# Optimization experiments

Measured on AMD Instinct MI355X. Metric: run time of the kernel, lower is better.

## Reference

```python
import jax, jax.numpy as jnp
import numpy as np

T, N, D = 64, 40, 4
H, R, K = 256, 64, 2
E = N * (N - 1)


def _xavier(key, shape):
    std = (2.0 / (shape[0] + shape[1])) ** 0.5
    return (std * jax.random.normal(key, shape)).astype(jnp.float32)


def setup_inputs() -> dict:
    ks = iter(jax.random.split(jax.random.key(0), 40))
    send, recv = np.where(np.ones((N, N)) - np.eye(N))  # fully-connected directed graph, E = N*(N-1)
    p = {}
    p['inputs'] = jax.random.normal(next(ks), (1, T, N, D), dtype=jnp.float32)
    p['node_masks'] = jnp.ones((1, T, N), dtype=jnp.float32)
    p['send_edges'] = jnp.asarray(send, dtype=jnp.int32)
    p['recv_edges'] = jnp.asarray(recv, dtype=jnp.int32)
    for name, nin in (('mlp1', D), ('mlp2', 2 * H), ('mlp3', H), ('mlp4', 3 * H)):
        p[name + '_W1'] = _xavier(next(ks), (H, nin))
        p[name + '_b1'] = jnp.full((H,), 0.1, jnp.float32)
        p[name + '_W2'] = _xavier(next(ks), (H, H))
        p[name + '_b2'] = jnp.full((H,), 0.1, jnp.float32)
    s = float(1.0 / np.sqrt(R))
    for nm in ('fwd', 'rev'):
        p[nm + '_Wih'] = jax.random.uniform(next(ks), (4 * R, H), jnp.float32, -s, s)
        p[nm + '_Whh'] = jax.random.uniform(next(ks), (4 * R, R), jnp.float32, -s, s)
        p[nm + '_bih'] = jnp.zeros((4 * R,), jnp.float32)
        p[nm + '_bhh'] = jnp.zeros((4 * R,), jnp.float32)
    p['enc_W'] = _xavier(next(ks), (K, 2 * R))
    p['enc_b'] = jnp.full((K,), 0.1, jnp.float32)
    p['prior_W'] = _xavier(next(ks), (K, R))
    p['prior_b'] = jnp.full((K,), 0.1, jnp.float32)
    return p


def _mlp(x, W1, b1, W2, b2):
    # RefNRIMLP in eval mode with no_bn=True: elu(fc2(elu(fc1(x))))
    return jax.nn.elu(jax.nn.elu(x @ W1.T + b1) @ W2.T + b2)


def _lstm(xs, Wih, Whh, bih, bhh):
    # xs: [T, E, H] -> hidden states [T, E, R]; PyTorch LSTM gate order i, f, g, o
    def step(carry, xt):
        h, c = carry
        g = xt @ Wih.T + bih + h @ Whh.T + bhh
        i, f, gg, o = jnp.split(g, 4, axis=-1)
        c = jax.nn.sigmoid(f) * c + jax.nn.sigmoid(i) * jnp.tanh(gg)
        h = jax.nn.sigmoid(o) * jnp.tanh(c)
        return (h, c), h
    Rh = Whh.shape[1]
    init = (jnp.zeros((xs.shape[1], Rh), xs.dtype), jnp.zeros((xs.shape[1], Rh), xs.dtype))
    _, hs = jax.lax.scan(step, init, xs)
    return hs


def _encode(inputs, send, recv,
            m1W1, m1b1, m1W2, m1b2, m2W1, m2b1, m2W2, m2b2,
            m3W1, m3b1, m3W2, m3b2, m4W1, m4b1, m4W2, m4b2,
            fWih, fWhh, fbih, fbhh, rWih, rWhh, rbih, rbhh,
            encW, encb, priW, prib):
    x = inputs[0]                                                  # [T, N, D]
    h = _mlp(x, m1W1, m1b1, m1W2, m1b2)                            # [T, N, H]
    e = jnp.concatenate([h[:, send], h[:, recv]], axis=-1)         # node2edge gather [T, E, 2H]
    e = _mlp(e, m2W1, m2b1, m2W2, m2b2)                            # [T, E, H]
    skip = e
    n = jnp.zeros((x.shape[0], x.shape[1], e.shape[-1]), e.dtype)
    n = n.at[:, recv].add(e)                                       # edge2node scatter-add (index_add_)
    n = _mlp(n, m3W1, m3b1, m3W2, m3b2)                            # [T, N, H]
    e = jnp.concatenate([n[:, send], n[:, recv], skip], axis=-1)   # [T, E, 3H]
    e = _mlp(e, m4W1, m4b1, m4W2, m4b2)                            # per-edge features over time [T, E, H]
    fwd_h = _lstm(e, fWih, fWhh, fbih, fbhh)                       # [T, E, R]
    rev_h = _lstm(e[::-1], rWih, rWhh, rbih, rbhh)[::-1]           # [T, E, R]
    prior = fwd_h @ priW.T + prib                                  # [T, E, K]
    enc = jnp.concatenate([fwd_h, rev_h], axis=-1) @ encW.T + encb # [T, E, K]
    return jnp.concatenate([prior, enc], axis=-1)                  # [T, E, 2K]


def reference(inputs, node_masks, send_edges, recv_edges,
              mlp1_W1, mlp1_b1, mlp1_W2, mlp1_b2,
              mlp2_W1, mlp2_b1, mlp2_W2, mlp2_b2,
              mlp3_W1, mlp3_b1, mlp3_W2, mlp3_b2,
              mlp4_W1, mlp4_b1, mlp4_W2, mlp4_b2,
              fwd_Wih, fwd_Whh, fwd_bih, fwd_bhh,
              rev_Wih, rev_Whh, rev_bih, rev_bhh,
              enc_W, enc_b, prior_W, prior_b):
    del node_masks  # all nodes present -> static fully-connected graph each step
    return _encode(inputs, send_edges, recv_edges,
                   mlp1_W1, mlp1_b1, mlp1_W2, mlp1_b2,
                   mlp2_W1, mlp2_b1, mlp2_W2, mlp2_b2,
                   mlp3_W1, mlp3_b1, mlp3_W2, mlp3_b2,
                   mlp4_W1, mlp4_b1, mlp4_W2, mlp4_b2,
                   fwd_Wih, fwd_Whh, fwd_bih, fwd_bhh,
                   rev_Wih, rev_Whh, rev_bih, rev_bhh,
                   enc_W, enc_b, prior_W, prior_b)
```

## Files before the change

kernel.cpp:

```cpp
#include <hip/hip_runtime.h>
#include <math.h>

#define T_ 64
#define N_ 40
#define D_ 4
#define H_ 256
#define R_ 64
#define E_ 1560
#define TE_ (T_*E_)
#define TN_ (T_*N_)

typedef unsigned short us;
typedef short short8 __attribute__((ext_vector_type(8)));
typedef float f32x4 __attribute__((ext_vector_type(4)));

__device__ __forceinline__ float elu_f(float x){ return x > 0.f ? x : (__expf(x) - 1.f); }
__device__ __forceinline__ float sig_f(float x){ return 1.f/(1.f+__expf(-x)); }
__device__ __forceinline__ float tanh_f(float x){ return 2.f/(1.f+__expf(-2.f*x)) - 1.f; }
__device__ __forceinline__ float dot4(float4 a, float4 b){ return a.x*b.x + a.y*b.y + a.z*b.z + a.w*b.w; }

__device__ __forceinline__ float bf2f(us u){ return __uint_as_float(((unsigned int)u) << 16); }
__device__ __forceinline__ us f2bf(float f){
    unsigned int u = __float_as_uint(f);
    u += 0x7FFFu + ((u >> 16) & 1u);
    return (us)(u >> 16);
}
__device__ __forceinline__ float4 ld4f(const float* p){ return *(const float4*)p; }
__device__ __forceinline__ float4 ld4f(const us* p){
    ushort4 v = *(const ushort4*)p;
    return make_float4(bf2f(v.x), bf2f(v.y), bf2f(v.z), bf2f(v.w));
}
__device__ __forceinline__ void st4f(float* p, float4 v){ *(float4*)p = v; }
__device__ __forceinline__ void st4f(us* p, float4 v){
    ushort4 o; o.x = f2bf(v.x); o.y = f2bf(v.y); o.z = f2bf(v.z); o.w = f2bf(v.w);
    *(ushort4*)p = o;
}

__device__ __forceinline__ void gld16(void* lds, const void* g){
    __builtin_amdgcn_global_load_lds((const __attribute__((address_space(1))) unsigned int*)g,
                                     (__attribute__((address_space(3))) unsigned int*)lds,
                                     16, 0, 0);
}

__device__ __forceinline__ void wsplit1(const float* W, us* hi, us* lo, int i){
    const float w = W[i];
    const us h = f2bf(w);
    hi[i] = h;
    lo[i] = f2bf(w - bf2f(h));
}

__global__ __launch_bounds__(256)
void wsplit_all(const float* __restrict__ s0, us* h0, us* l0,
                const float* __restrict__ s1, us* h1, us* l1,
                const float* __restrict__ s2, us* h2, us* l2,
                const float* __restrict__ s3, us* h3, us* l3,
                const float* __restrict__ s4, us* h4, us* l4,
                const float* __restrict__ s5, us* h5, us* l5,
                const float* __restrict__ s6, us* h6, us* l6,
                const float* __restrict__ s7, us* h7, us* l7)
{
    int i = blockIdx.x * 256 + threadIdx.x;
    if (i < 131072) { wsplit1(s0, h0, l0, i); return; } i -= 131072;
    if (i <  65536) { wsplit1(s1, h1, l1, i); return; } i -=  65536;
    if (i < 196608) { wsplit1(s2, h2, l2, i); return; } i -= 196608;
    if (i <  65536) { wsplit1(s3, h3, l3, i); return; } i -=  65536;
    if (i <  65536) { wsplit1(s4, h4, l4, i); return; } i -=  65536;
    if (i <  65536) { wsplit1(s5, h5, l5, i); return; } i -=  65536;
    if (i <  16384) { wsplit1(s6, h6, l6, i); return; } i -=  16384;
    wsplit1(s7, h7, l7, i);
}

__global__ __launch_bounds__(256)
void mlp1_kernel(const float* __restrict__ x,
                 const float* __restrict__ W1, const float* __restrict__ b1,
                 const float* __restrict__ W2, const float* __restrict__ b2,
                 us* __restrict__ hout)
{
    __shared__ float xs[8][4];
    __shared__ float h1[8][256];
    const int tid = threadIdx.x;
    const int r0  = blockIdx.x * 8;

    if (tid < 32) xs[tid >> 2][tid & 3] = x[r0 * 4 + tid];
    __syncthreads();

    const float4 w1 = *(const float4*)&W1[tid * 4];
    const float bb1 = b1[tid];
    #pragma unroll
    for (int row = 0; row < 8; ++row) {
        float v = bb1 + xs[row][0]*w1.x + xs[row][1]*w1.y + xs[row][2]*w1.z + xs[row][3]*w1.w;
        h1[row][tid] = elu_f(v);
    }
    __syncthreads();

    float acc[8];
    const float bb2 = b2[tid];
    #pragma unroll
    for (int row = 0; row < 8; ++row) acc[row] = bb2;
    const float* w2row = W2 + (size_t)tid * 256;
    for (int k4 = 0; k4 < 64; ++k4) {
        const float4 w = *(const float4*)&w2row[k4 * 4];
        #pragma unroll
        for (int row = 0; row < 8; ++row) {
            const float4 hh = *(const float4*)&h1[row][k4 * 4];
            acc[row] += dot4(hh, w);
        }
    }
    #pragma unroll
    for (int row = 0; row < 8; ++row)
        hout[(size_t)(r0 + row) * 256 + tid] = f2bf(elu_f(acc[row]));
}

template<int MODE, bool DOELU>
__global__ __launch_bounds__(256)
void gemm_mfma(const us* __restrict__ A, const us* __restrict__ A2, const us* __restrict__ A3,
               const us* __restrict__ Whi, const us* __restrict__ Wlo,
               const float* __restrict__ bias1, const float* __restrict__ bias2,
               const int* __restrict__ send, const int* __restrict__ recv,
               us* __restrict__ C, int Kdim,
               const us* __restrict__ Whi2, const us* __restrict__ Wlo2,
               const float* __restrict__ bias1b, const float* __restrict__ bias2b,
               us* __restrict__ C2)
{
    __shared__ char smem[49152];

    const int tid  = threadIdx.x;
    const int lane = tid & 63;
    const int w    = tid >> 6;
    const int ml   = lane & 15;
    const int q    = lane >> 4;
    const int bx   = blockIdx.x;
    int by         = blockIdx.y;
    const int eh   = w >> 1;
    const int fh   = w & 1;

    if (MODE == 0 && C2 != nullptr && by >= 2) {
        Whi = Whi2; Wlo = Wlo2; bias1 = bias1b; bias2 = bias2b; C = C2; by -= 2;
    }

    const int srow0 = w * 32 + (lane >> 2);
    const int srow1 = srow0 + 16;
    const int cofs  = (lane & 3) * 8;

    const int gr0 = bx * 128 + srow0, gr1 = bx * 128 + srow1;
    const us *pA0a=nullptr,*pA1a=nullptr,*pA2a=nullptr;
    const us *pA0b=nullptr,*pA1b=nullptr,*pA2b=nullptr;
    if (MODE == 0) {
        pA0a = A + (size_t)gr0 * Kdim;
        pA0b = A + (size_t)gr1 * Kdim;
    } else {
        const int t0 = gr0 / E_, e0 = gr0 - t0 * E_;
        const int t1 = gr1 / E_, e1 = gr1 - t1 * E_;
        pA0a = A  + ((size_t)(t0 * N_ + send[e0])) * H_;
        pA1a = A2 + ((size_t)(t0 * N_ + recv[e0])) * H_;
        pA0b = A  + ((size_t)(t1 * N_ + send[e1])) * H_;
        pA1b = A2 + ((size_t)(t1 * N_ + recv[e1])) * H_;
        if (MODE == 2) { pA2a = A3 + (size_t)gr0 * H_; pA2b = A3 + (size_t)gr1 * H_; }
    }
    const us* pWh0 = Whi + (size_t)(by * 128 + srow0) * Kdim;
    const us* pWh1 = Whi + (size_t)(by * 128 + srow1) * Kdim;
    const us* pWl0 = Wlo + (size_t)(by * 128 + srow0) * Kdim;
    const us* pWl1 = Wlo + (size_t)(by * 128 + srow1) * Kdim;

    f32x4 acc[4][4];
    #pragma unroll
    for (int i = 0; i < 4; ++i)
        #pragma unroll
        for (int j = 0; j < 4; ++j)
            acc[i][j] = (f32x4){0.f, 0.f, 0.f, 0.f};

    auto stage = [&](int k0, char* base) {
        const us *sa, *sb;
        if (MODE == 0) { sa = pA0a + k0; sb = pA0b + k0; }
        else if (MODE == 1) {
            sa = (k0 < 256) ? pA0a + k0 : pA1a + (k0 - 256);
            sb = (k0 < 256) ? pA0b + k0 : pA1b + (k0 - 256);
        } else {
            sa = (k0 < 256) ? pA0a + k0 : (k0 < 512) ? pA1a + (k0 - 256) : pA2a + (k0 - 512);
            sb = (k0 < 256) ? pA0b + k0 : (k0 < 512) ? pA1b + (k0 - 256) : pA2b + (k0 - 512);
        }
        gld16(base + w * 2048,                sa + cofs);
        gld16(base + w * 2048 + 1024,         sb + cofs);
        gld16(base + 8192  + w * 2048,        pWh0 + k0 + cofs);
        gld16(base + 8192  + w * 2048 + 1024, pWh1 + k0 + cofs);
        gld16(base + 16384 + w * 2048,        pWl0 + k0 + cofs);
        gld16(base + 16384 + w * 2048 + 1024, pWl1 + k0 + cofs);
    };

    stage(0, smem);
    const int nk = Kdim >> 5;
    for (int k = 0; k < nk; ++k) {
        char* cur = smem + (k & 1) * 24576;
        char* nxt = smem + ((k + 1) & 1) * 24576;
        __builtin_amdgcn_s_barrier();
        if (k + 1 < nk) {
            stage((k + 1) * 32, nxt);
            __builtin_amdgcn_s_waitcnt(0x3F76);
        } else {
            __builtin_amdgcn_s_waitcnt(0x3F70);
        }
        __builtin_amdgcn_s_barrier();

        short8 wh[4], wl[4], ef[4];
        #pragma unroll
        for (int mt = 0; mt < 4; ++mt) {
            const int fr = fh * 64 + mt * 16 + ml;
            wh[mt] = *(const short8*)(cur + 8192  + fr * 64 + q * 16);
            wl[mt] = *(const short8*)(cur + 16384 + fr * 64 + q * 16);
        }
        #pragma unroll
        for (int nt = 0; nt < 4; ++nt) {
            const int er = eh * 64 + nt * 16 + ml;
            ef[nt] = *(const short8*)(cur + er * 64 + q * 16);
        }
        #pragma unroll
        for (int mt = 0; mt < 4; ++mt)
            #pragma unroll
            for (int nt = 0; nt < 4; ++nt) {
                acc[mt][nt] = __builtin_amdgcn_mfma_f32_16x16x32_bf16(wh[mt], ef[nt], acc[mt][nt], 0, 0, 0);
                acc[mt][nt] = __builtin_amdgcn_mfma_f32_16x16x32_bf16(wl[mt], ef[nt], acc[mt][nt], 0, 0, 0);
            }
    }

    #pragma unroll
    for (int mt = 0; mt < 4; ++mt) {
        const int colb = by * 128 + fh * 64 + mt * 16 + q * 4;
        float4 bb = *(const float4*)(bias1 + colb);
        if (bias2) {
            const float4 b2 = *(const float4*)(bias2 + colb);
            bb.x += b2.x; bb.y += b2.y; bb.z += b2.z; bb.w += b2.w;
        }
        #pragma unroll
        for (int nt = 0; nt < 4; ++nt) {
            const int row = bx * 128 + eh * 64 + nt * 16 + ml;
            float4 v;
            v.x = acc[mt][nt][0] + bb.x; v.y = acc[mt][nt][1] + bb.y;
            v.z = acc[mt][nt][2] + bb.z; v.w = acc[mt][nt][3] + bb.w;
            if (DOELU) { v.x = elu_f(v.x); v.y = elu_f(v.y); v.z = elu_f(v.z); v.w = elu_f(v.w); }
            ushort4 o; o.x = f2bf(v.x); o.y = f2bf(v.y); o.z = f2bf(v.z); o.w = f2bf(v.w);
            *(ushort4*)(C + (size_t)row * 256 + colb) = o;
        }
    }
}

template<bool DOELU, typename TA, typename TC>
__global__ __launch_bounds__(256)
void gemm_nt(const TA* __restrict__ A, const float* __restrict__ W,
             const float* __restrict__ bias1,
             TC* __restrict__ C, int M, int Kdim)
{
    __shared__ float As[16][64];
    __shared__ float Ws[16][64];

    const int tid = threadIdx.x;
    const int am  = tid >> 2;
    const int ak  = (tid & 3) * 4;
    const int gm  = blockIdx.x * 64 + am;

    const TA* aptr0 = A + (size_t)gm * Kdim;
    const float* wptr = W + (size_t)(blockIdx.y * 64 + am) * Kdim;

    const int tx = tid & 15, ty = tid >> 4;
    float acc[4][4] = {};

    for (int k0 = 0; k0 < Kdim; k0 += 16) {
        const float4 a4 = ld4f(aptr0 + k0 + ak);
        const float4 w4 = *(const float4*)(wptr + k0 + (tid & 3) * 4);

        __syncthreads();
        As[ak+0][am] = a4.x; As[ak+1][am] = a4.y; As[ak+2][am] = a4.z; As[ak+3][am] = a4.w;
        const int wk = (tid & 3) * 4;
        Ws[wk+0][am] = w4.x; Ws[wk+1][am] = w4.y; Ws[wk+2][am] = w4.z; Ws[wk+3][am] = w4.w;
        __syncthreads();

        #pragma unroll
        for (int kq = 0; kq < 16; ++kq) {
            const float4 av = *(const float4*)&As[kq][ty * 4];
            const float4 wv = *(const float4*)&Ws[kq][tx * 4];
            const float a_[4] = {av.x, av.y, av.z, av.w};
            const float w_[4] = {wv.x, wv.y, wv.z, wv.w};
            #pragma unroll
            for (int i = 0; i < 4; ++i)
                #pragma unroll
                for (int j = 0; j < 4; ++j)
                    acc[i][j] += a_[i] * w_[j];
        }
    }

    const int gn = blockIdx.y * 64 + tx * 4;
    const float4 bb = *(const float4*)&bias1[gn];
    #pragma unroll
    for (int i = 0; i < 4; ++i) {
        const int row = blockIdx.x * 64 + ty * 4 + i;
        float4 o;
        o.x = acc[i][0] + bb.x; o.y = acc[i][1] + bb.y;
        o.z = acc[i][2] + bb.z; o.w = acc[i][3] + bb.w;
        if (DOELU) { o.x = elu_f(o.x); o.y = elu_f(o.y); o.z = elu_f(o.z); o.w = elu_f(o.w); }
        st4f(C + (size_t)row * 256 + gn, o);
    }
}

__global__ __launch_bounds__(256)
void aggregate_kernel(const us* __restrict__ eSkip, const int* __restrict__ recv,
                      float* __restrict__ nAgg)
{
    const int t = blockIdx.x / N_;
    const int j = blockIdx.x - t * N_;
    const int c = threadIdx.x;
    const us* basep = eSkip + (size_t)t * E_ * H_ + c;
    float acc = 0.f;
    #pragma unroll
    for (int s = 0; s < N_; ++s) {
        if (s == j) continue;
        const int e = s * (N_ - 1) + (j < s ? j : j - 1);
        acc += bf2f(basep[(size_t)e * H_]);
    }
    nAgg[(size_t)blockIdx.x * H_ + c] = acc;
}

__global__ __launch_bounds__(256)
void lstm_mfma(const us* __restrict__ Gf, const us* __restrict__ Gr,
               const us* __restrict__ fWhhH, const us* __restrict__ fWhhL,
               const us* __restrict__ rWhhH, const us* __restrict__ rWhhL,
               float* __restrict__ hsF, float* __restrict__ hsR)
{
    const int NBD = (E_ + 15) / 16;
    const bool revd = (int)blockIdx.x >= NBD;
    const int blk = revd ? (int)blockIdx.x - NBD : (int)blockIdx.x;
    const int e0 = blk * 16;
    const us* G  = revd ? Gr : Gf;
    const us* WH = revd ? rWhhH : fWhhH;
    const us* WL = revd ? rWhhL : fWhhL;
    float* hs    = revd ? hsR : hsF;

    const int tid  = threadIdx.x;
    const int lane = tid & 63;
    const int w    = tid >> 6;
    const int ml   = lane & 15;
    const int q    = lane >> 4;

    __shared__ float g_s[4][16][68];
    __shared__ us hHi[16][72];
    __shared__ us hLo[16][72];

    short8 wfh[4][2], wfl[4][2];
    #pragma unroll
    for (int mt = 0; mt < 4; ++mt) {
        const int row = w * 64 + mt * 16 + ml;
        #pragma unroll
        for (int ks = 0; ks < 2; ++ks) {
            wfh[mt][ks] = *(const short8*)(WH + (size_t)row * 64 + ks * 32 + q * 8);
            wfl[mt][ks] = *(const short8*)(WL + (size_t)row * 64 + ks * 32 + q * 8);
        }
    }

    for (int i = tid; i < 16 * 72; i += 256) { ((us*)hHi)[i] = 0; ((us*)hLo)[i] = 0; }

    const int ped = tid >> 4;
    const int prr = (tid & 15) * 4;
    float4 cst = make_float4(0.f, 0.f, 0.f, 0.f);

    const int eMF = min(e0 + ml, E_ - 1);
    const int gb  = w * 64 + q * 4;

    ushort4 gcur[4], gnxt[4];
    {
        const int tt0 = revd ? (T_ - 1) : 0;
        const us* gp = G + ((size_t)tt0 * E_ + eMF) * 256 + gb;
        #pragma unroll
        for (int mt = 0; mt < 4; ++mt) gcur[mt] = *(const ushort4*)(gp + mt * 16);
    }
    __syncthreads();

    for (int s = 0; s < T_; ++s) {
        const int tt = revd ? (T_ - 1 - s) : s;
        {
            const int sn = (s + 1 < T_) ? s + 1 : s;
            const int tn = revd ? (T_ - 1 - sn) : sn;
            const us* gp = G + ((size_t)tn * E_ + eMF) * 256 + gb;
            #pragma unroll
            for (int mt = 0; mt < 4; ++mt) gnxt[mt] = *(const ushort4*)(gp + mt * 16);
        }
        short8 bh[2], bl[2];
        #pragma unroll
        for (int ks = 0; ks < 2; ++ks) {
            bh[ks] = *(const short8*)(&hHi[ml][ks * 32 + q * 8]);
            bl[ks] = *(const short8*)(&hLo[ml][ks * 32 + q * 8]);
        }
        #pragma unroll
        for (int mt = 0; mt < 4; ++mt) {
            f32x4 acc;
            acc[0] = bf2f(gcur[mt].x); acc[1] = bf2f(gcur[mt].y);
            acc[2] = bf2f(gcur[mt].z); acc[3] = bf2f(gcur[mt].w);
            #pragma unroll
            for (int ks = 0; ks < 2; ++ks) {
                acc = __builtin_amdgcn_mfma_f32_16x16x32_bf16(wfh[mt][ks], bh[ks], acc, 0, 0, 0);
                acc = __builtin_amdgcn_mfma_f32_16x16x32_bf16(wfh[mt][ks], bl[ks], acc, 0, 0, 0);
                acc = __builtin_amdgcn_mfma_f32_16x16x32_bf16(wfl[mt][ks], bh[ks], acc, 0, 0, 0);
            }
            *(f32x4*)(&g_s[w][ml][mt * 16 + q * 4]) = acc;
        }
        __syncthreads();
        {
            const float4 gi = *(const float4*)&g_s[0][ped][prr];
            const float4 gf = *(const float4*)&g_s[1][ped][prr];
            const float4 gg = *(const float4*)&g_s[2][ped][prr];
            const float4 go = *(const float4*)&g_s[3][ped][prr];
            float4 hv;
            cst.x = sig_f(gf.x)*cst.x + sig_f(gi.x)*tanh_f(gg.x); hv.x = sig_f(go.x)*tanh_f(cst.x);
            cst.y = sig_f(gf.y)*cst.y + sig_f(gi.y)*tanh_f(gg.y); hv.y = sig_f(go.y)*tanh_f(cst.y);
            cst.z = sig_f(gf.z)*cst.z + sig_f(gi.z)*tanh_f(gg.z); hv.z = sig_f(go.z)*tanh_f(cst.z);
            cst.w = sig_f(gf.w)*cst.w + sig_f(gi.w)*tanh_f(gg.w); hv.w = sig_f(go.w)*tanh_f(cst.w);
            ushort4 hh4, hl4;
            hh4.x = f2bf(hv.x); hl4.x = f2bf(hv.x - bf2f(hh4.x));
            hh4.y = f2bf(hv.y); hl4.y = f2bf(hv.y - bf2f(hh4.y));
            hh4.z = f2bf(hv.z); hl4.z = f2bf(hv.z - bf2f(hh4.z));
            hh4.w = f2bf(hv.w); hl4.w = f2bf(hv.w - bf2f(hh4.w));
            *(ushort4*)(&hHi[ped][prr]) = hh4;
            *(ushort4*)(&hLo[ped][prr]) = hl4;
            if (e0 + ped < E_)
                *(float4*)(&hs[((size_t)tt * E_ + e0 + ped) * 64 + prr]) = hv;
        }
        __syncthreads();
        #pragma unroll
        for (int mt = 0; mt < 4; ++mt) gcur[mt] = gnxt[mt];
    }
}

__global__ __launch_bounds__(256)
void out_kernel(const float* __restrict__ hsF, const float* __restrict__ hsR,
                const float* __restrict__ priW, const float* __restrict__ prib,
                const float* __restrict__ encW, const float* __restrict__ encb,
                float* __restrict__ out)
{
    const int idx = blockIdx.x * 256 + threadIdx.x;
    const float* f = hsF + (size_t)idx * 64;
    const float* r = hsR + (size_t)idx * 64;
    float p0 = prib[0], p1 = prib[1], q0 = encb[0], q1 = encb[1];
    #pragma unroll
    for (int k4 = 0; k4 < 16; ++k4) {
        const float4 fv = *(const float4*)(f + k4 * 4);
        const float4 rv = *(const float4*)(r + k4 * 4);
        p0 += dot4(fv, *(const float4*)(priW + k4 * 4));
        p1 += dot4(fv, *(const float4*)(priW + 64 + k4 * 4));
        q0 += dot4(fv, *(const float4*)(encW + k4 * 4))
            + dot4(rv, *(const float4*)(encW + 64 + k4 * 4));
        q1 += dot4(fv, *(const float4*)(encW + 128 + k4 * 4))
            + dot4(rv, *(const float4*)(encW + 192 + k4 * 4));
    }
    float4 o; o.x = p0; o.y = p1; o.z = q0; o.w = q1;
    *(float4*)(out + (size_t)idx * 4) = o;
}

extern "C" void kernel_launch(void* const* d_in, const int* in_sizes, int n_in,
                              void* d_out, int out_size, void* d_ws, size_t ws_size,
                              hipStream_t stream)
{
    const float* x    = (const float*)d_in[0];
    const int*   send = (const int*)d_in[2];
    const int*   recv = (const int*)d_in[3];
    const float* m1W1 = (const float*)d_in[4];  const float* m1b1 = (const float*)d_in[5];
    const float* m1W2 = (const float*)d_in[6];  const float* m1b2 = (const float*)d_in[7];
    const float* m2W1 = (const float*)d_in[8];  const float* m2b1 = (const float*)d_in[9];
    const float* m2W2 = (const float*)d_in[10]; const float* m2b2 = (const float*)d_in[11];
    const float* m3W1 = (const float*)d_in[12]; const float* m3b1 = (const float*)d_in[13];
    const float* m3W2 = (const float*)d_in[14]; const float* m3b2 = (const float*)d_in[15];
    const float* m4W1 = (const float*)d_in[16]; const float* m4b1 = (const float*)d_in[17];
    const float* m4W2 = (const float*)d_in[18]; const float* m4b2 = (const float*)d_in[19];
    const float* fWih = (const float*)d_in[20]; const float* fWhh = (const float*)d_in[21];
    const float* fbih = (const float*)d_in[22]; const float* fbhh = (const float*)d_in[23];
    const float* rWih = (const float*)d_in[24]; const float* rWhh = (const float*)d_in[25];
    const float* rbih = (const float*)d_in[26]; const float* rbhh = (const float*)d_in[27];
    const float* encW = (const float*)d_in[28]; const float* encb = (const float*)d_in[29];
    const float* priW = (const float*)d_in[30]; const float* prib = (const float*)d_in[31];

    const size_t SZN  = (size_t)TN_ * H_;
    const size_t SZE  = (size_t)TE_ * H_;
    float* n_agg = (float*)d_ws;
    float* m3t   = n_agg + SZN;
    us* h16      = (us*)(m3t + SZN);
    us* n3       = h16 + SZN;
    us* w2aH = n3  + SZN;          us* w2aL = w2aH + 256*512;
    us* w2bH = w2aL + 256*512;     us* w2bL = w2bH + 256*256;
    us* w4aH = w2bL + 256*256;     us* w4aL = w4aH + 256*768;
    us* w4bH = w4aL + 256*768;     us* w4bL = w4bH + 256*256;
    us* wfiH = w4bL + 256*256;     us* wfiL = wfiH + 256*256;
    us* wriH = wfiL + 256*256;     us* wriL = wriH + 256*256;
    us* whfH = wriL + 256*256;     us* whfL = whfH + 256*64;
    us* whrH = whfL + 256*64;      us* whrL = whrH + 256*64;
    us* bufA16 = whrL + 256*64;
    us* bufB16 = bufA16 + SZE;
    us* bufC16 = bufB16 + SZE;
    float* hsF = (float*)bufC16;
    float* hsR = hsF + (size_t)TE_ * R_;
    const size_t needed = ((size_t)(bufC16 + SZE) - (size_t)d_ws);
    if (ws_size < needed) return;

    const dim3 gMF(TE_ / 128, 2), gMF4(TE_ / 128, 4), gN(TN_ / 64, 4);
    const us* z = nullptr; const float* zf = nullptr; us* zo = nullptr;

    wsplit_all<<<2432, 256, 0, stream>>>(m2W1, w2aH, w2aL, m2W2, w2bH, w2bL,
                                         m4W1, w4aH, w4aL, m4W2, w4bH, w4bL,
                                         fWih, wfiH, wfiL, rWih, wriH, wriL,
                                         fWhh, whfH, whfL, rWhh, whrH, whrL);

    mlp1_kernel<<<TN_ / 8, 256, 0, stream>>>(x, m1W1, m1b1, m1W2, m1b2, h16);
    gemm_mfma<1, true><<<gMF, 256, 0, stream>>>(h16, h16, nullptr, w2aH, w2aL, m2b1, nullptr, send, recv, bufA16, 512, z, z, zf, zf, zo);
    gemm_mfma<0, true><<<gMF, 256, 0, stream>>>(bufA16, nullptr, nullptr, w2bH, w2bL, m2b2, nullptr, send, recv, bufB16, 256, z, z, zf, zf, zo);
    aggregate_kernel<<<TN_, 256, 0, stream>>>(bufB16, recv, n_agg);
    gemm_nt<true, float, float><<<gN, 256, 0, stream>>>(n_agg, m3W1, m3b1, m3t, TN_, 256);
    gemm_nt<true, float, us><<<gN, 256, 0, stream>>>(m3t, m3W2, m3b2, n3, TN_, 256);
    gemm_mfma<2, true><<<gMF, 256, 0, stream>>>(n3, n3, bufB16, w4aH, w4aL, m4b1, nullptr, send, recv, bufA16, 768, z, z, zf, zf, zo);
    gemm_mfma<0, true><<<gMF, 256, 0, stream>>>(bufA16, nullptr, nullptr, w4bH, w4bL, m4b2, nullptr, send, recv, bufC16, 256, z, z, zf, zf, zo);
    gemm_mfma<0, false><<<gMF4, 256, 0, stream>>>(bufC16, nullptr, nullptr, wfiH, wfiL, fbih, fbhh, send, recv, bufA16, 256,
                                                  wriH, wriL, rbih, rbhh, bufB16);
    lstm_mfma<<<2 * ((E_ + 15) / 16), 256, 0, stream>>>(bufA16, bufB16, whfH, whfL, whrH, whrL, hsF, hsR);
    out_kernel<<<TE_ / 256, 256, 0, stream>>>(hsF, hsR, priW, prib, encW, encb, (float*)d_out);
}
```

Baseline: 604.3 us.

## Keep LSTM gates in registers and double-buffer hidden state to drop a barrier

The LSTM recurrence kernel reassigns Whh rows so each wave holds all four gates (i,f,g,o) for the same 16 hidden units. The cell update can then run straight from the MFMA accumulators, with no round trip through a shared gate buffer. The hidden state is double-buffered in shared memory, so each timestep needs one barrier instead of two. The GEMM kernel's shared-memory staging layout also changes to a blocked fragment order, likely to reduce LDS bank conflicts on fragment reads.

```diff
diff --git a/kernel.cpp b/kernel.cpp
--- a/kernel.cpp
+++ b/kernel.cpp
@@ -138,9 +138,9 @@
         Whi = Whi2; Wlo = Wlo2; bias1 = bias1b; bias2 = bias2b; C = C2; by -= 2;
     }
 
-    const int srow0 = w * 32 + (lane >> 2);
+    const int srow0 = w * 32 + ml;
     const int srow1 = srow0 + 16;
-    const int cofs  = (lane & 3) * 8;
+    const int cofs  = q * 8;
 
     const int gr0 = bx * 128 + srow0, gr1 = bx * 128 + srow1;
     const us *pA0a=nullptr,*pA1a=nullptr,*pA2a=nullptr;
@@ -204,14 +204,14 @@
         short8 wh[4], wl[4], ef[4];
         #pragma unroll
         for (int mt = 0; mt < 4; ++mt) {
-            const int fr = fh * 64 + mt * 16 + ml;
-            wh[mt] = *(const short8*)(cur + 8192  + fr * 64 + q * 16);
-            wl[mt] = *(const short8*)(cur + 16384 + fr * 64 + q * 16);
+            const int blkOf = (fh * 4 + mt) * 1024 + q * 256 + ml * 16;
+            wh[mt] = *(const short8*)(cur + 8192  + blkOf);
+            wl[mt] = *(const short8*)(cur + 16384 + blkOf);
         }
         #pragma unroll
         for (int nt = 0; nt < 4; ++nt) {
-            const int er = eh * 64 + nt * 16 + ml;
-            ef[nt] = *(const short8*)(cur + er * 64 + q * 16);
+            const int blkOf = (eh * 4 + nt) * 1024 + q * 256 + ml * 16;
+            ef[nt] = *(const short8*)(cur + blkOf);
         }
         #pragma unroll
         for (int mt = 0; mt < 4; ++mt)
@@ -339,14 +339,13 @@
     const int ml   = lane & 15;
     const int q    = lane >> 4;
 
-    __shared__ float g_s[4][16][68];
-    __shared__ us hHi[16][72];
-    __shared__ us hLo[16][72];
+    __shared__ us hHi[2][16][72];
+    __shared__ us hLo[2][16][72];
 
     short8 wfh[4][2], wfl[4][2];
     #pragma unroll
     for (int mt = 0; mt < 4; ++mt) {
-        const int row = w * 64 + mt * 16 + ml;
+        const int row = mt * 64 + w * 16 + ml;
         #pragma unroll
         for (int ks = 0; ks < 2; ++ks) {
             wfh[mt][ks] = *(const short8*)(WH + (size_t)row * 64 + ks * 32 + q * 8);
@@ -354,21 +353,19 @@
         }
     }
 
-    for (int i = tid; i < 16 * 72; i += 256) { ((us*)hHi)[i] = 0; ((us*)hLo)[i] = 0; }
-
-    const int ped = tid >> 4;
-    const int prr = (tid & 15) * 4;
+    for (int i = tid; i < 16 * 72; i += 256) { (&hHi[0][0][0])[i] = 0; (&hLo[0][0][0])[i] = 0; }
+
+    const int eMF = min(e0 + ml, E_ - 1);
+    const bool wr = (e0 + ml) < E_;
+    const int gOfs = w * 16 + q * 4;
     float4 cst = make_float4(0.f, 0.f, 0.f, 0.f);
-
-    const int eMF = min(e0 + ml, E_ - 1);
-    const int gb  = w * 64 + q * 4;
 
     ushort4 gcur[4], gnxt[4];
     {
         const int tt0 = revd ? (T_ - 1) : 0;
-        const us* gp = G + ((size_t)tt0 * E_ + eMF) * 256 + gb;
-        #pragma unroll
-        for (int mt = 0; mt < 4; ++mt) gcur[mt] = *(const ushort4*)(gp + mt * 16);
+        const us* gp = G + ((size_t)tt0 * E_ + eMF) * 256 + gOfs;
+        #pragma unroll
+        for (int mt = 0; mt < 4; ++mt) gcur[mt] = *(const ushort4*)(gp + mt * 64);
     }
     __syncthreads();
 
@@ -377,50 +374,43 @@
         {
             const int sn = (s + 1 < T_) ? s + 1 : s;
             const int tn = revd ? (T_ - 1 - sn) : sn;
-            const us* gp = G + ((size_t)tn * E_ + eMF) * 256 + gb;
+            const us* gp = G + ((size_t)tn * E_ + eMF) * 256 + gOfs;
             #pragma unroll
-            for (int mt = 0; mt < 4; ++mt) gnxt[mt] = *(const ushort4*)(gp + mt * 16);
-        }
+            for (int mt = 0; mt < 4; ++mt) gnxt[mt] = *(const ushort4*)(gp + mt * 64);
+        }
+        const int rb = s & 1, wb = rb ^ 1;
         short8 bh[2], bl[2];
         #pragma unroll
         for (int ks = 0; ks < 2; ++ks) {
-            bh[ks] = *(const short8*)(&hHi[ml][ks * 32 + q * 8]);
-            bl[ks] = *(const short8*)(&hLo[ml][ks * 32 + q * 8]);
-        }
+            bh[ks] = *(const short8*)(&hHi[rb][ml][ks * 32 + q * 8]);
+            bl[ks] = *(const short8*)(&hLo[rb][ml][ks * 32 + q * 8]);
+        }
+        f32x4 acc[4];
         #pragma unroll
         for (int mt = 0; mt < 4; ++mt) {
-            f32x4 acc;
-            acc[0] = bf2f(gcur[mt].x); acc[1] = bf2f(gcur[mt].y);
-            acc[2] = bf2f(gcur[mt].z); acc[3] = bf2f(gcur[mt].w);
+            acc[mt][0] = bf2f(gcur[mt].x); acc[mt][1] = bf2f(gcur[mt].y);
+            acc[mt][2] = bf2f(gcur[mt].z); acc[mt][3] = bf2f(gcur[mt].w);
             #pragma unroll
             for (int ks = 0; ks < 2; ++ks) {
-                acc = __builtin_amdgcn_mfma_f32_16x16x32_bf16(wfh[mt][ks], bh[ks], acc, 0, 0, 0);
-                acc = __builtin_amdgcn_mfma_f32_16x16x32_bf16(wfh[mt][ks], bl[ks], acc, 0, 0, 0);
-                acc = __builtin_amdgcn_mfma_f32_16x16x32_bf16(wfl[mt][ks], bh[ks], acc, 0, 0, 0);
+                acc[mt] = __builtin_amdgcn_mfma_f32_16x16x32_bf16(wfh[mt][ks], bh[ks], acc[mt], 0, 0, 0);
+                acc[mt] = __builtin_amdgcn_mfma_f32_16x16x32_bf16(wfh[mt][ks], bl[ks], acc[mt], 0, 0, 0);
+                acc[mt] = __builtin_amdgcn_mfma_f32_16x16x32_bf16(wfl[mt][ks], bh[ks], acc[mt], 0, 0, 0);
             }
-            *(f32x4*)(&g_s[w][ml][mt * 16 + q * 4]) = acc;
-        }
-        __syncthreads();
-        {
-            const float4 gi = *(const float4*)&g_s[0][ped][prr];
-            const float4 gf = *(const float4*)&g_s[1][ped][prr];
-            const float4 gg = *(const float4*)&g_s[2][ped][prr];
-            const float4 go = *(const float4*)&g_s[3][ped][prr];
-            float4 hv;
-            cst.x = sig_f(gf.x)*cst.x + sig_f(gi.x)*tanh_f(gg.x); hv.x = sig_f(go.x)*tanh_f(cst.x);
-            cst.y = sig_f(gf.y)*cst.y + sig_f(gi.y)*tanh_f(gg.y); hv.y = sig_f(go.y)*tanh_f(cst.y);
-            cst.z = sig_f(gf.z)*cst.z + sig_f(gi.z)*tanh_f(gg.z); hv.z = sig_f(go.z)*tanh_f(cst.z);
-            cst.w = sig_f(gf.w)*cst.w + sig_f(gi.w)*tanh_f(gg.w); hv.w = sig_f(go.w)*tanh_f(cst.w);
-            ushort4 hh4, hl4;
-            hh4.x = f2bf(hv.x); hl4.x = f2bf(hv.x - bf2f(hh4.x));
-            hh4.y = f2bf(hv.y); hl4.y = f2bf(hv.y - bf2f(hh4.y));
-            hh4.z = f2bf(hv.z); hl4.z = f2bf(hv.z - bf2f(hh4.z));
-            hh4.w = f2bf(hv.w); hl4.w = f2bf(hv.w - bf2f(hh4.w));
-            *(ushort4*)(&hHi[ped][prr]) = hh4;
-            *(ushort4*)(&hLo[ped][prr]) = hl4;
-            if (e0 + ped < E_)
-                *(float4*)(&hs[((size_t)tt * E_ + e0 + ped) * 64 + prr]) = hv;
-        }
+        }
+        float4 hv;
+        cst.x = sig_f(acc[1][0])*cst.x + sig_f(acc[0][0])*tanh_f(acc[2][0]); hv.x = sig_f(acc[3][0])*tanh_f(cst.x);
+        cst.y = sig_f(acc[1][1])*cst.y + sig_f(acc[0][1])*tanh_f(acc[2][1]); hv.y = sig_f(acc[3][1])*tanh_f(cst.y);
+        cst.z = sig_f(acc[1][2])*cst.z + sig_f(acc[0][2])*tanh_f(acc[2][2]); hv.z = sig_f(acc[3][2])*tanh_f(cst.z);
+        cst.w = sig_f(acc[1][3])*cst.w + sig_f(acc[0][3])*tanh_f(acc[2][3]); hv.w = sig_f(acc[3][3])*tanh_f(cst.w);
+        ushort4 hh4, hl4;
+        hh4.x = f2bf(hv.x); hl4.x = f2bf(hv.x - bf2f(hh4.x));
+        hh4.y = f2bf(hv.y); hl4.y = f2bf(hv.y - bf2f(hh4.y));
+        hh4.z = f2bf(hv.z); hl4.z = f2bf(hv.z - bf2f(hh4.z));
+        hh4.w = f2bf(hv.w); hl4.w = f2bf(hv.w - bf2f(hh4.w));
+        *(ushort4*)(&hHi[wb][ml][gOfs]) = hh4;
+        *(ushort4*)(&hLo[wb][ml][gOfs]) = hl4;
+        if (wr)
+            *(float4*)(&hs[((size_t)tt * E_ + e0 + ml) * 64 + gOfs]) = hv;
         __syncthreads();
         #pragma unroll
         for (int mt = 0; mt < 4; ++mt) gcur[mt] = gnxt[mt];
```

Measured after the change: 667.4 us. 1.1x slower.
